# Kernel optimization log

Hardware: AMD Instinct MI355X
Metric: run time of the kernel (lower is better)

Reference implementation:

```python
import jax, jax.numpy as jnp
import numpy as np

N = 50000        # nodes
E = 800000       # edges
G = 256          # graphs in batch
DIMS = [128, 128, 64, 32]
BN_EPS = 1e-5
TEMP = 5.0


def setup_inputs() -> dict:
    key = jax.random.key(0)
    ks = iter(jax.random.split(key, 32))
    inp = {}
    inp["x"] = jax.random.normal(next(ks), (N, DIMS[0]), dtype=jnp.float32)
    inp["edge_index"] = jax.random.randint(next(ks), (2, E), 0, N)
    inp["batch"] = jnp.sort(jax.random.randint(next(ks), (N,), 0, G))
    for i in range(3):
        din, dout = DIMS[i], DIMS[i + 1]
        inp[f"W1_{i}"] = jax.random.normal(next(ks), (din, dout), dtype=jnp.float32) * 0.05
        inp[f"b1_{i}"] = jnp.zeros((dout,), jnp.float32)
        inp[f"W2_{i}"] = jax.random.normal(next(ks), (dout, dout), dtype=jnp.float32) * 0.05
        inp[f"b2_{i}"] = jnp.zeros((dout,), jnp.float32)
        inp[f"gamma_{i}"] = jnp.ones((dout,), jnp.float32)
        inp[f"beta_{i}"] = jnp.zeros((dout,), jnp.float32)
        inp[f"mean_{i}"] = jnp.zeros((dout,), jnp.float32)
        inp[f"var_{i}"] = jnp.ones((dout,), jnp.float32)
    inp["W_lin"] = jax.random.normal(next(ks), (DIMS[3], 1), dtype=jnp.float32) * 0.05
    inp["b_lin"] = jnp.zeros((1,), jnp.float32)
    return inp


def _gin_bn(x, src, dst, W1, b1, W2, b2, g, b, m, v):
    # GINConv with eps=0: h_i = MLP(x_i + sum_{j->i} x_j), then BatchNorm (eval)
    agg = jax.ops.segment_sum(x[src], dst, num_segments=N)  # [N, din]
    h = x + agg
    h = jnp.maximum(h @ W1 + b1, 0.0) @ W2 + b2             # 2-layer MLP
    return (h - m) * jax.lax.rsqrt(v + BN_EPS) * g + b


def reference(x, edge_index, batch,
              W1_0, b1_0, W2_0, b2_0, gamma_0, beta_0, mean_0, var_0,
              W1_1, b1_1, W2_1, b2_1, gamma_1, beta_1, mean_1, var_1,
              W1_2, b1_2, W2_2, b2_2, gamma_2, beta_2, mean_2, var_2,
              W_lin, b_lin):
    src, dst = edge_index[0], edge_index[1]
    layers = [
        (W1_0, b1_0, W2_0, b2_0, gamma_0, beta_0, mean_0, var_0),
        (W1_1, b1_1, W2_1, b2_1, gamma_1, beta_1, mean_1, var_1),
        (W1_2, b1_2, W2_2, b2_2, gamma_2, beta_2, mean_2, var_2),
    ]
    for i, p in enumerate(layers):
        x = _gin_bn(x, src, dst, *p)
        if i != len(layers) - 1:
            x = jnp.maximum(x, 0.0)  # relu; dropout is identity in eval mode
    logits = (x @ W_lin + b_lin) / TEMP                      # [N, 1]
    # per-graph (segment) softmax over nodes
    mx = jax.ops.segment_max(logits, batch, num_segments=G)  # [G, 1]
    e = jnp.exp(logits - mx[batch])
    s = jax.ops.segment_sum(e, batch, num_segments=G)        # [G, 1]
    return e / s[batch]
```

## Files before the change

kernel.cpp:

```cpp
#include <hip/hip_runtime.h>

#define NN 50000
#define NE 800000
#define NG 256
#define NB ((NN + 255) / 256)
#define N4 (NN * 128 / 4)

typedef __attribute__((ext_vector_type(8))) short bf16x8;
typedef __attribute__((ext_vector_type(4))) float f32x4;

__device__ __forceinline__ unsigned short f2bf_rne(float f) {
    unsigned u = __float_as_uint(f);
    u += 0x7fffu + ((u >> 16) & 1u);
    return (unsigned short)(u >> 16);
}
#define BF2F_LO(u) __uint_as_float((u) << 16)
#define BF2F_HI(u) __uint_as_float((u) & 0xffff0000u)

__global__ void conv_hist(const float4* __restrict__ x, ushort4* __restrict__ xh,
                          const int* __restrict__ dst, int* __restrict__ deg,
                          int* __restrict__ eoff) {
    int i = blockIdx.x * 256 + threadIdx.x;
    if (i < N4) {
        float4 v = x[i];
        ushort4 o;
        o.x = f2bf_rne(v.x); o.y = f2bf_rne(v.y);
        o.z = f2bf_rne(v.z); o.w = f2bf_rne(v.w);
        xh[i] = o;
    }
    if (i < NE) eoff[i] = atomicAdd(&deg[dst[i]], 1);
}

__global__ void block_scan(const int* __restrict__ deg, int* __restrict__ iscan,
                           int* __restrict__ bsum,
                           const float* __restrict__ W1, const float* __restrict__ W2,
                           const float* __restrict__ W3,
                           unsigned short* __restrict__ W1t,
                           unsigned short* __restrict__ W2t,
                           unsigned short* __restrict__ W3t) {
    int gidx = blockIdx.x * 256 + threadIdx.x;
    if (gidx < 16384) {
        int n = gidx >> 7, k = gidx & 127;
        W1t[gidx] = f2bf_rne(W1[k * 128 + n]);
        W2t[gidx] = f2bf_rne(W2[k * 128 + n]);
    } else if (gidx < 24576) {
        int i2 = gidx - 16384;
        int n = i2 >> 7, k = i2 & 127;
        W3t[i2] = f2bf_rne(W3[k * 64 + n]);
    }

    __shared__ int sh[256];
    int t = threadIdx.x;
    int i = blockIdx.x * 256 + t;
    int v = (i < NN) ? deg[i] : 0;
    sh[t] = v;
    __syncthreads();
    #pragma unroll
    for (int off = 1; off < 256; off <<= 1) {
        int add = (t >= off) ? sh[t - off] : 0;
        __syncthreads();
        sh[t] += add;
        __syncthreads();
    }
    if (i < NN) iscan[i] = sh[t];
    if (t == 255) bsum[blockIdx.x] = sh[255];
}

__global__ void scan_bsum(const int* __restrict__ bsum, int* __restrict__ boff) {
    __shared__ int sh[256];
    int t = threadIdx.x;
    int v = (t < NB) ? bsum[t] : 0;
    sh[t] = v;
    __syncthreads();
    #pragma unroll
    for (int off = 1; off < 256; off <<= 1) {
        int add = (t >= off) ? sh[t - off] : 0;
        __syncthreads();
        sh[t] += add;
        __syncthreads();
    }
    if (t < NB) boff[t] = sh[t] - v;
}

__global__ void finalize_bounds(const int* __restrict__ deg, const int* __restrict__ iscan,
                                const int* __restrict__ boff, int* __restrict__ rowptr,
                                const int* __restrict__ batch, int* __restrict__ gstart) {
    int i = blockIdx.x * 256 + threadIdx.x;
    if (i < NN) {
        rowptr[i] = iscan[i] - deg[i] + boff[blockIdx.x];
        int b = batch[i];
        if (i == 0) {
            for (int g = 0; g <= b; g++) gstart[g] = 0;
        } else {
            int p = batch[i - 1];
            for (int g = p + 1; g <= b; g++) gstart[g] = i;
        }
        if (i == NN - 1) {
            for (int g = b + 1; g <= NG; g++) gstart[g] = NN;
        }
    }
    if (i == 0) rowptr[NN] = NE;
}

__global__ void fill_csr2(const int* __restrict__ src, const int* __restrict__ dst,
                          const int* __restrict__ rowptr, const int* __restrict__ eoff,
                          int* __restrict__ esrc) {
    int e = blockIdx.x * blockDim.x + threadIdx.x;
    if (e >= NE) return;
    esrc[rowptr[dst[e]] + eoff[e]] = src[e];
}


template <int C4>
__device__ __forceinline__ void gather_bf16(const uint4* __restrict__ x4,
                                            const int* __restrict__ esrc,
                                            int beg, int cnt, int node, int lane,
                                            float* a ) {
    constexpr int EPI = 64 / C4;
    const int chunk = lane & (C4 - 1);
    const int esl   = lane / C4;
    #define ACC_U4(u) do { \
        a[0] += BF2F_LO((u).x); a[1] += BF2F_HI((u).x); \
        a[2] += BF2F_LO((u).y); a[3] += BF2F_HI((u).y); \
        a[4] += BF2F_LO((u).z); a[5] += BF2F_HI((u).z); \
        a[6] += BF2F_LO((u).w); a[7] += BF2F_HI((u).w); } while (0)
    if (esl == 0) { uint4 u = x4[(size_t)node * C4 + chunk]; ACC_U4(u); }
    for (int c = 0; c < cnt; c += 64) {
        int take = min(64, cnt - c);
        int myi = (lane < take) ? esrc[beg + c + lane] : 0;
        int i = 0;
        for (; i + 4 * EPI <= take; i += 4 * EPI) {
            int s0 = __shfl(myi, i + esl);
            int s1 = __shfl(myi, i + EPI + esl);
            int s2 = __shfl(myi, i + 2 * EPI + esl);
            int s3 = __shfl(myi, i + 3 * EPI + esl);
            uint4 u0 = x4[(size_t)s0 * C4 + chunk];
            uint4 u1 = x4[(size_t)s1 * C4 + chunk];
            uint4 u2 = x4[(size_t)s2 * C4 + chunk];
            uint4 u3 = x4[(size_t)s3 * C4 + chunk];
            ACC_U4(u0); ACC_U4(u1); ACC_U4(u2); ACC_U4(u3);
        }
        if (i + 2 * EPI <= take) {
            int s0 = __shfl(myi, i + esl);
            int s1 = __shfl(myi, i + EPI + esl);
            uint4 u0 = x4[(size_t)s0 * C4 + chunk];
            uint4 u1 = x4[(size_t)s1 * C4 + chunk];
            ACC_U4(u0); ACC_U4(u1);
            i += 2 * EPI;
        }
        if (i + EPI <= take) {
            int s = __shfl(myi, i + esl);
            uint4 u = x4[(size_t)s * C4 + chunk];
            ACC_U4(u);
            i += EPI;
        }
        int rem = take - i;
        if (rem > 0) {
            int s = __shfl(myi, i + ((esl < rem) ? esl : 0));
            uint4 u = x4[(size_t)s * C4 + chunk];
            if (esl < rem) ACC_U4(u);
        }
    }
    #undef ACC_U4
    for (int off = 32; off >= C4; off >>= 1) {
        #pragma unroll
        for (int q = 0; q < 8; q++)
            a[q] += __shfl_xor(a[q], off);
    }
}

template <int C>
__device__ __forceinline__ void gather_bf16_u2(const uint2* __restrict__ x2,
                                               const int* __restrict__ esrc,
                                               int beg, int cnt, int node, int lane,
                                               float* a ) {
    constexpr int EPI = 64 / C;
    const int chunk = lane & (C - 1);
    const int esl   = lane / C;
    #define ACC_U2(u) do { \
        a[0] += BF2F_LO((u).x); a[1] += BF2F_HI((u).x); \
        a[2] += BF2F_LO((u).y); a[3] += BF2F_HI((u).y); } while (0)
    if (esl == 0) { uint2 u = x2[(size_t)node * C + chunk]; ACC_U2(u); }
    for (int c = 0; c < cnt; c += 64) {
        int take = min(64, cnt - c);
        int myi = (lane < take) ? esrc[beg + c + lane] : 0;
        int i = 0;
        for (; i + 4 * EPI <= take; i += 4 * EPI) {
            int s0 = __shfl(myi, i + esl);
            int s1 = __shfl(myi, i + EPI + esl);
            int s2 = __shfl(myi, i + 2 * EPI + esl);
            int s3 = __shfl(myi, i + 3 * EPI + esl);
            uint2 u0 = x2[(size_t)s0 * C + chunk];
            uint2 u1 = x2[(size_t)s1 * C + chunk];
            uint2 u2 = x2[(size_t)s2 * C + chunk];
            uint2 u3 = x2[(size_t)s3 * C + chunk];
            ACC_U2(u0); ACC_U2(u1); ACC_U2(u2); ACC_U2(u3);
        }
        if (i + 2 * EPI <= take) {
            int s0 = __shfl(myi, i + esl);
            int s1 = __shfl(myi, i + EPI + esl);
            uint2 u0 = x2[(size_t)s0 * C + chunk];
            uint2 u1 = x2[(size_t)s1 * C + chunk];
            ACC_U2(u0); ACC_U2(u1);
            i += 2 * EPI;
        }
        if (i + EPI <= take) {
            int s = __shfl(myi, i + esl);
            uint2 u = x2[(size_t)s * C + chunk];
            ACC_U2(u);
            i += EPI;
        }
        int rem = take - i;
        if (rem > 0) {
            int s = __shfl(myi, i + ((esl < rem) ? esl : 0));
            uint2 u = x2[(size_t)s * C + chunk];
            if (esl < rem) ACC_U2(u);
        }
    }
    #undef ACC_U2
    for (int off = 32; off >= C; off >>= 1) {
        #pragma unroll
        for (int q = 0; q < 4; q++)
            a[q] += __shfl_xor(a[q], off);
    }
}

template <int C>
__device__ __forceinline__ void gather_bf16_u1(const unsigned* __restrict__ x1,
                                               const int* __restrict__ esrc,
                                               int beg, int cnt, int node, int lane,
                                               float* a ) {
    constexpr int EPI = 64 / C;
    const int chunk = lane & (C - 1);
    const int esl   = lane / C;
    #define ACC_U1(u) do { \
        a[0] += BF2F_LO(u); a[1] += BF2F_HI(u); } while (0)
    if (esl == 0) { unsigned u = x1[(size_t)node * C + chunk]; ACC_U1(u); }
    for (int c = 0; c < cnt; c += 64) {
        int take = min(64, cnt - c);
        int myi = (lane < take) ? esrc[beg + c + lane] : 0;
        int i = 0;
        for (; i + 4 * EPI <= take; i += 4 * EPI) {
            int s0 = __shfl(myi, i + esl);
            int s1 = __shfl(myi, i + EPI + esl);
            int s2 = __shfl(myi, i + 2 * EPI + esl);
            int s3 = __shfl(myi, i + 3 * EPI + esl);
            unsigned u0 = x1[(size_t)s0 * C + chunk];
            unsigned u1 = x1[(size_t)s1 * C + chunk];
            unsigned u2 = x1[(size_t)s2 * C + chunk];
            unsigned u3 = x1[(size_t)s3 * C + chunk];
            ACC_U1(u0); ACC_U1(u1); ACC_U1(u2); ACC_U1(u3);
        }
        if (i + 2 * EPI <= take) {
            int s0 = __shfl(myi, i + esl);
            int s1 = __shfl(myi, i + EPI + esl);
            unsigned u0 = x1[(size_t)s0 * C + chunk];
            unsigned u1 = x1[(size_t)s1 * C + chunk];
            ACC_U1(u0); ACC_U1(u1);
            i += 2 * EPI;
        }
        if (i + EPI <= take) {
            int s = __shfl(myi, i + esl);
            unsigned u = x1[(size_t)s * C + chunk];
            ACC_U1(u);
            i += EPI;
        }
        int rem = take - i;
        if (rem > 0) {
            int s = __shfl(myi, i + ((esl < rem) ? esl : 0));
            unsigned u = x1[(size_t)s * C + chunk];
            if (esl < rem) ACC_U1(u);
        }
    }
    #undef ACC_U1
    for (int off = 32; off >= C; off >>= 1) {
        #pragma unroll
        for (int q = 0; q < 2; q++)
            a[q] += __shfl_xor(a[q], off);
    }
}

__global__ __launch_bounds__(256) void gather_L0(
        const unsigned short* __restrict__ xh, const int* __restrict__ esrc,
        const int* __restrict__ rowptr, unsigned short* __restrict__ aggh ) {
    const int wave = threadIdx.x >> 6, lane = threadIdx.x & 63;
    const int node = blockIdx.x * 4 + wave;
    if (node >= NN) return;
    float a[8] = {0, 0, 0, 0, 0, 0, 0, 0};
    int beg = rowptr[node], end = rowptr[node + 1];
    gather_bf16<16>((const uint4*)xh, esrc, beg, end - beg, node, lane, a);
    if (lane < 16) {
        uint4 o;
        o.x = (unsigned)f2bf_rne(a[0]) | ((unsigned)f2bf_rne(a[1]) << 16);
        o.y = (unsigned)f2bf_rne(a[2]) | ((unsigned)f2bf_rne(a[3]) << 16);
        o.z = (unsigned)f2bf_rne(a[4]) | ((unsigned)f2bf_rne(a[5]) << 16);
        o.w = (unsigned)f2bf_rne(a[6]) | ((unsigned)f2bf_rne(a[7]) << 16);
        *(uint4*)&aggh[(size_t)node * 128 + lane * 8] = o;
    }
}

__global__ __launch_bounds__(256) void gemm_L0(
        const unsigned short* __restrict__ aggh, unsigned short* __restrict__ z1h,
        const unsigned short* __restrict__ W1t,
        const unsigned short* __restrict__ W2t,
        const unsigned short* __restrict__ W3t,
        const float* __restrict__ b1, const float* __restrict__ b2,
        const float* __restrict__ gamma, const float* __restrict__ beta,
        const float* __restrict__ mean, const float* __restrict__ var) {
    constexpr int MT = 64, LDA = 136;
    __shared__ __align__(16) unsigned short shA[MT * LDA];
    __shared__ __align__(16) unsigned short shB[MT * LDA];
    const int tid = threadIdx.x;
    const int wave = tid >> 6, lane = tid & 63;
    const int nodeBase = blockIdx.x * MT;
    const int lr = lane & 15;
    const int lg = lane >> 4;
    const int lk = lg * 8;
    const int n0 = wave * 32;

    #pragma unroll
    for (int j = 0; j < 4; j++) {
        int f = tid + j * 256;
        int row = f >> 4, c = f & 15;
        int node = nodeBase + row;
        uint4 v = (node < NN) ? ((const uint4*)aggh)[(size_t)node * 16 + c]
                              : make_uint4(0u, 0u, 0u, 0u);
        *(uint4*)&shA[row * LDA + c * 8] = v;
    }
    __syncthreads();

    f32x4 acc[4][2];

    {
        float bv0 = b1[n0 + lr], bv1 = b1[n0 + 16 + lr];
        #pragma unroll
        for (int m = 0; m < 4; m++) {
            f32x4 c0 = {bv0, bv0, bv0, bv0};
            f32x4 c1 = {bv1, bv1, bv1, bv1};
            acc[m][0] = c0; acc[m][1] = c1;
        }
        #pragma unroll
        for (int ks = 0; ks < 4; ks++) {
            const int k0 = ks * 32 + lk;
            bf16x8 wb0 = *(const bf16x8*)&W1t[(n0 + lr) * 128 + k0];
            bf16x8 wb1 = *(const bf16x8*)&W1t[(n0 + 16 + lr) * 128 + k0];
            #pragma unroll
            for (int m = 0; m < 4; m++) {
                bf16x8 af = *(const bf16x8*)&shA[(m * 16 + lr) * LDA + k0];
                acc[m][0] = __builtin_amdgcn_mfma_f32_16x16x32_bf16(af, wb0, acc[m][0], 0, 0, 0);
                acc[m][1] = __builtin_amdgcn_mfma_f32_16x16x32_bf16(af, wb1, acc[m][1], 0, 0, 0);
            }
        }
    }
    #pragma unroll
    for (int m = 0; m < 4; m++) {
        #pragma unroll
        for (int nt = 0; nt < 2; nt++) {
            #pragma unroll
            for (int r = 0; r < 4; r++) {
                shB[(m * 16 + lg * 4 + r) * LDA + (n0 + nt * 16 + lr)] =
                    f2bf_rne(fmaxf(acc[m][nt][r], 0.f));
            }
        }
    }
    __syncthreads();

    {
        float bv0 = b2[n0 + lr], bv1 = b2[n0 + 16 + lr];
        #pragma unroll
        for (int m = 0; m < 4; m++) {
            f32x4 c0 = {bv0, bv0, bv0, bv0};
            f32x4 c1 = {bv1, bv1, bv1, bv1};
            acc[m][0] = c0; acc[m][1] = c1;
        }
        #pragma unroll
        for (int ks = 0; ks < 4; ks++) {
            const int k0 = ks * 32 + lk;
            bf16x8 wb0 = *(const bf16x8*)&W2t[(n0 + lr) * 128 + k0];
            bf16x8 wb1 = *(const bf16x8*)&W2t[(n0 + 16 + lr) * 128 + k0];
            #pragma unroll
            for (int m = 0; m < 4; m++) {
                bf16x8 af = *(const bf16x8*)&shB[(m * 16 + lr) * LDA + k0];
                acc[m][0] = __builtin_amdgcn_mfma_f32_16x16x32_bf16(af, wb0, acc[m][0], 0, 0, 0);
                acc[m][1] = __builtin_amdgcn_mfma_f32_16x16x32_bf16(af, wb1, acc[m][1], 0, 0, 0);
            }
        }
    }
    float s0 = gamma[n0 + lr]      * (1.0f / sqrtf(var[n0 + lr] + 1e-5f));
    float t0 = beta[n0 + lr]       - mean[n0 + lr] * s0;
    float s1 = gamma[n0 + 16 + lr] * (1.0f / sqrtf(var[n0 + 16 + lr] + 1e-5f));
    float t1 = beta[n0 + 16 + lr]  - mean[n0 + 16 + lr] * s1;
    #pragma unroll
    for (int m = 0; m < 4; m++) {
        #pragma unroll
        for (int nt = 0; nt < 2; nt++) {
            float sc = nt ? s1 : s0, sf = nt ? t1 : t0;
            #pragma unroll
            for (int r = 0; r < 4; r++) {
                float y = fmaxf(fmaf(acc[m][nt][r], sc, sf), 0.f);
                shA[(m * 16 + lg * 4 + r) * LDA + (n0 + nt * 16 + lr)] = f2bf_rne(y);
            }
        }
    }
    __syncthreads();

    f32x4 a3[4];
    #pragma unroll
    for (int m = 0; m < 4; m++) {
        f32x4 z = {0.f, 0.f, 0.f, 0.f};
        a3[m] = z;
    }
    #pragma unroll
    for (int ks = 0; ks < 4; ks++) {
        const int k0 = ks * 32 + lk;
        bf16x8 wb = *(const bf16x8*)&W3t[(wave * 16 + lr) * 128 + k0];
        #pragma unroll
        for (int m = 0; m < 4; m++) {
            bf16x8 af = *(const bf16x8*)&shA[(m * 16 + lr) * LDA + k0];
            a3[m] = __builtin_amdgcn_mfma_f32_16x16x32_bf16(af, wb, a3[m], 0, 0, 0);
        }
    }
    #pragma unroll
    for (int m = 0; m < 4; m++) {
        #pragma unroll
        for (int r = 0; r < 4; r++) {
            int node = nodeBase + m * 16 + lg * 4 + r;
            if (node < NN)
                z1h[(size_t)node * 64 + wave * 16 + lr] = f2bf_rne(a3[m][r]);
        }
    }
}

__global__ __launch_bounds__(256) void fused_L1(
        const unsigned short* __restrict__ z1h, const int* __restrict__ esrc,
        const int* __restrict__ rowptr, unsigned short* __restrict__ z2h,
        const float* __restrict__ b1, const float* __restrict__ W2,
        const float* __restrict__ b2, const float* __restrict__ gamma,
        const float* __restrict__ beta, const float* __restrict__ mean,
        const float* __restrict__ var, const float* __restrict__ Wn ) {
    constexpr int MT = 32, LD = 68;
    __shared__ float sh[MT * LD];
    const int tid = threadIdx.x, wave = tid >> 6, lane = tid & 63;
    const int nodeBase = blockIdx.x * MT;

    for (int r = wave; r < MT; r += 4) {
        int node = nodeBase + r;
        float a[4] = {0, 0, 0, 0};
        if (node < NN) {
            int beg = rowptr[node], end = rowptr[node + 1];
            gather_bf16_u2<16>((const uint2*)z1h, esrc, beg, end - beg, node, lane, a);
        }
        if (lane < 16) {
            float4 b0 = *(const float4*)&b1[lane * 4];
            *(float4*)&sh[r * LD + lane * 4] = make_float4(
                fmaxf(a[0] + b0.x, 0.f), fmaxf(a[1] + b0.y, 0.f),
                fmaxf(a[2] + b0.z, 0.f), fmaxf(a[3] + b0.w, 0.f));
        }
    }
    __syncthreads();

    const int colid = tid % 16, rowid = tid / 16;
    const int c0 = colid * 4, r0 = rowid * 2;
    float acc[2][4];
    {
        float4 bv = *(const float4*)&b2[c0];
        #pragma unroll
        for (int i = 0; i < 2; i++) {
            acc[i][0] = bv.x; acc[i][1] = bv.y; acc[i][2] = bv.z; acc[i][3] = bv.w;
        }
        #pragma unroll 2
        for (int k4 = 0; k4 < 16; k4++) {
            float4 w[4];
            #pragma unroll
            for (int kk = 0; kk < 4; kk++)
                w[kk] = *(const float4*)&W2[(k4 * 4 + kk) * 64 + c0];
            #pragma unroll
            for (int i = 0; i < 2; i++) {
                float4 a = *(const float4*)&sh[(r0 + i) * LD + k4 * 4];
                const float av[4] = {a.x, a.y, a.z, a.w};
                #pragma unroll
                for (int kk = 0; kk < 4; kk++) {
                    const float* wp = (const float*)&w[kk];
                    #pragma unroll
                    for (int j = 0; j < 4; j++)
                        acc[i][j] = fmaf(av[kk], wp[j], acc[i][j]);
                }
            }
        }
    }
    float4 gv = *(const float4*)&gamma[c0];
    float4 bev = *(const float4*)&beta[c0];
    float4 mv = *(const float4*)&mean[c0];
    float4 vv = *(const float4*)&var[c0];
    float scale[4], shift[4];
    {
        const float* gp = (const float*)&gv; const float* bp = (const float*)&bev;
        const float* mp = (const float*)&mv; const float* vp = (const float*)&vv;
        #pragma unroll
        for (int j = 0; j < 4; j++) {
            scale[j] = gp[j] * (1.0f / sqrtf(vp[j] + 1e-5f));
            shift[j] = bp[j] - mp[j] * scale[j];
        }
    }
    __syncthreads();
    #pragma unroll
    for (int i = 0; i < 2; i++) {
        float4 y;
        y.x = fmaxf(fmaf(acc[i][0], scale[0], shift[0]), 0.f);
        y.y = fmaxf(fmaf(acc[i][1], scale[1], shift[1]), 0.f);
        y.z = fmaxf(fmaf(acc[i][2], scale[2], shift[2]), 0.f);
        y.w = fmaxf(fmaf(acc[i][3], scale[3], shift[3]), 0.f);
        *(float4*)&sh[(r0 + i) * LD + c0] = y;
    }
    __syncthreads();

    {
        const int colid2 = tid % 8, rowid2 = tid / 8;
        const int c0b = colid2 * 4, r0b = rowid2;
        float a3[4] = {};
        #pragma unroll 2
        for (int k4 = 0; k4 < 16; k4++) {
            float4 w[4];
            #pragma unroll
            for (int kk = 0; kk < 4; kk++)
                w[kk] = *(const float4*)&Wn[(k4 * 4 + kk) * 32 + c0b];
            float4 a = *(const float4*)&sh[r0b * LD + k4 * 4];
            const float av[4] = {a.x, a.y, a.z, a.w};
            #pragma unroll
            for (int kk = 0; kk < 4; kk++) {
                const float* wp = (const float*)&w[kk];
                #pragma unroll
                for (int j = 0; j < 4; j++)
                    a3[j] = fmaf(av[kk], wp[j], a3[j]);
            }
        }
        int node = nodeBase + r0b;
        if (node < NN) {
            ushort4 o;
            o.x = f2bf_rne(a3[0]); o.y = f2bf_rne(a3[1]);
            o.z = f2bf_rne(a3[2]); o.w = f2bf_rne(a3[3]);
            *(ushort4*)&z2h[(size_t)node * 32 + c0b] = o;
        }
    }
}

__global__ __launch_bounds__(256) void fused_L2(
        const unsigned short* __restrict__ z2h, const int* __restrict__ esrc,
        const int* __restrict__ rowptr, float* __restrict__ logits,
        const float* __restrict__ b1, const float* __restrict__ W2,
        const float* __restrict__ b2, const float* __restrict__ gamma,
        const float* __restrict__ beta, const float* __restrict__ mean,
        const float* __restrict__ var, const float* __restrict__ Wl,
        const float* __restrict__ bl) {
    constexpr int MT = 32, LD = 36;
    __shared__ float sh[MT * LD];
    const int tid = threadIdx.x, wave = tid >> 6, lane = tid & 63;
    const int nodeBase = blockIdx.x * MT;

    for (int r = wave; r < MT; r += 4) {
        int node = nodeBase + r;
        float a[2] = {0, 0};
        if (node < NN) {
            int beg = rowptr[node], end = rowptr[node + 1];
            gather_bf16_u1<16>((const unsigned*)z2h, esrc, beg, end - beg, node, lane, a);
        }
        if (lane < 16) {
            float2 bv = *(const float2*)&b1[lane * 2];
            *(float2*)&sh[r * LD + lane * 2] = make_float2(
                fmaxf(a[0] + bv.x, 0.f), fmaxf(a[1] + bv.y, 0.f));
        }
    }
    __syncthreads();

    const int colid = tid % 8, rowid = tid / 8;
    const int c0 = colid * 4, r0 = rowid;
    float acc[4];
    {
        float4 bv = *(const float4*)&b2[c0];
        acc[0] = bv.x; acc[1] = bv.y; acc[2] = bv.z; acc[3] = bv.w;
        #pragma unroll
        for (int k4 = 0; k4 < 8; k4++) {
            float4 w[4];
            #pragma unroll
            for (int kk = 0; kk < 4; kk++)
                w[kk] = *(const float4*)&W2[(k4 * 4 + kk) * 32 + c0];
            float4 a = *(const float4*)&sh[r0 * LD + k4 * 4];
            const float av[4] = {a.x, a.y, a.z, a.w};
            #pragma unroll
            for (int kk = 0; kk < 4; kk++) {
                const float* wp = (const float*)&w[kk];
                #pragma unroll
                for (int j = 0; j < 4; j++)
                    acc[j] = fmaf(av[kk], wp[j], acc[j]);
            }
        }
    }
    float4 gv = *(const float4*)&gamma[c0];
    float4 bev = *(const float4*)&beta[c0];
    float4 mv = *(const float4*)&mean[c0];
    float4 vv = *(const float4*)&var[c0];
    float4 wl = *(const float4*)&Wl[c0];
    float p = 0.f;
    {
        const float* gp = (const float*)&gv; const float* bp = (const float*)&bev;
        const float* mp = (const float*)&mv; const float* vp = (const float*)&vv;
        const float* wp = (const float*)&wl;
        #pragma unroll
        for (int j = 0; j < 4; j++) {
            float sc = gp[j] * (1.0f / sqrtf(vp[j] + 1e-5f));
            float y = (acc[j] - mp[j]) * sc + bp[j];
            p = fmaf(y, wp[j], p);
        }
    }
    p += __shfl_xor(p, 1);
    p += __shfl_xor(p, 2);
    p += __shfl_xor(p, 4);
    int node = nodeBase + r0;
    if ((tid & 7) == 0 && node < NN)
        logits[node] = (p + bl[0]) * 0.2f;
}

__global__ __launch_bounds__(256) void seg_softmax(
        const float* __restrict__ logits, const int* __restrict__ gstart,
        float* __restrict__ out) {
    __shared__ float slog[1024];
    __shared__ float sred[4];
    __shared__ float sbc[2];
    int g = blockIdx.x;
    int beg = gstart[g], end = gstart[g + 1];
    int cnt = end - beg;
    int t = threadIdx.x;
    if (cnt <= 0) return;
    bool fits = (cnt <= 1024);

    float lmax = -3.402823466e+38f;
    for (int i = t; i < cnt; i += 256) {
        float lg = logits[beg + i];
        if (fits) slog[i] = lg;
        lmax = fmaxf(lmax, lg);
    }
    #pragma unroll
    for (int off = 32; off > 0; off >>= 1)
        lmax = fmaxf(lmax, __shfl_down(lmax, off));
    if ((t & 63) == 0) sred[t >> 6] = lmax;
    __syncthreads();
    if (t == 0) sbc[0] = fmaxf(fmaxf(sred[0], sred[1]), fmaxf(sred[2], sred[3]));
    __syncthreads();
    float gm = sbc[0];

    float lsum = 0.f;
    for (int i = t; i < cnt; i += 256) {
        float lg = fits ? slog[i] : logits[beg + i];
        float e = expf(lg - gm);
        if (fits) slog[i] = e;
        lsum += e;
    }
    #pragma unroll
    for (int off = 32; off > 0; off >>= 1)
        lsum += __shfl_down(lsum, off);
    __syncthreads();
    if ((t & 63) == 0) sred[t >> 6] = lsum;
    __syncthreads();
    if (t == 0) sbc[1] = (sred[0] + sred[1]) + (sred[2] + sred[3]);
    __syncthreads();
    float inv = 1.0f / sbc[1];

    for (int i = t; i < cnt; i += 256) {
        float e = fits ? slog[i] : expf(logits[beg + i] - gm);
        out[beg + i] = e * inv;
    }
}

extern "C" void kernel_launch(void* const* d_in, const int* in_sizes, int n_in,
                              void* d_out, int out_size, void* d_ws, size_t ws_size,
                              hipStream_t stream) {
    const float* x    = (const float*)d_in[0];
    const int*   ei   = (const int*)d_in[1];
    const int*   srcI = ei;
    const int*   dstI = ei + NE;
    const int*   batch = (const int*)d_in[2];

    const float* P[29];
    for (int i = 0; i < 29; i++) P[i] = (const float*)d_in[i];
    const float* Wlin = P[27];
    const float* blin = P[28];

    unsigned short* xh  = (unsigned short*)d_ws;
    unsigned short* z1h = xh + (size_t)NN * 128;
    unsigned short* z2h = z1h + (size_t)NN * 64;
    float* logits = (float*)(z2h + (size_t)NN * 32);
    int* gstart = (int*)(logits + NN);
    int* deg    = gstart + NG + 1;
    int* iscan  = deg + NN;
    int* rowptr = iscan + NN;
    int* bsum   = rowptr + NN + 1;
    int* boff   = bsum + NB;
    int* eoff   = boff + NB;
    int* esrc   = eoff + NE;
    uintptr_t pal = ((uintptr_t)(esrc + NE) + 255) & ~(uintptr_t)255;
    unsigned short* aggh = (unsigned short*)pal;
    unsigned short* W1t  = aggh + (size_t)NN * 128;
    unsigned short* W2t  = W1t + 16384;
    unsigned short* W3t  = W2t + 16384;
    float* outp = (float*)d_out;

    const int TB = 256;

    hipMemsetAsync(deg, 0, NN * sizeof(int), stream);
    conv_hist<<<(N4 + TB - 1) / TB, TB, 0, stream>>>(
        (const float4*)x, (ushort4*)xh, dstI, deg, eoff);

    block_scan<<<NB, 256, 0, stream>>>(deg, iscan, bsum,
        P[3], P[5], P[11], W1t, W2t, W3t);
    scan_bsum<<<1, 256, 0, stream>>>(bsum, boff);
    finalize_bounds<<<NB, 256, 0, stream>>>(deg, iscan, boff, rowptr, batch, gstart);
    fill_csr2<<<(NE + TB - 1) / TB, TB, 0, stream>>>(srcI, dstI, rowptr, eoff, esrc);

    const int GB  = (NN + 3) / 4;
    const int FB64 = (NN + 63) / 64;
    const int FB32 = (NN + 31) / 32;

    gather_L0<<<GB, 256, 0, stream>>>(xh, esrc, rowptr, aggh);
    gemm_L0<<<FB64, 256, 0, stream>>>(aggh, z1h, W1t, W2t, W3t,
        P[4], P[6], P[7], P[8], P[9], P[10]);
    fused_L1<<<FB32, 256, 0, stream>>>(z1h, esrc, rowptr, z2h,
        P[12], P[13], P[14], P[15], P[16], P[17], P[18], P[19]);
    fused_L2<<<FB32, 256, 0, stream>>>(z2h, esrc, rowptr, logits,
        P[20], P[21], P[22], P[23], P[24], P[25], P[26], Wlin, blin);

    seg_softmax<<<NG, 256, 0, stream>>>(logits, gstart, outp);
}
```

Before: 305.6 us.

## Split L1/L2 fused kernels into gather + MFMA GEMM kernels

The fused gather-plus-FP32-GEMM kernels for layers 1 and 2 are each split into a separate per-node gather kernel and a dense GEMM kernel. The gathers write bf16 aggregates to new workspace buffers. The layer-1 MLP now runs on bf16 MFMA instructions using weights transposed and converted in the setup kernel, replacing scalar FP32 FMAs. This is meant to cut ALU time and stop the gather latency from stalling the GEMM. The cost is extra global round trips for the intermediates, two more kernel launches, and bf16 rounding of the layer-1 GEMM inputs.

```diff
diff --git a/kernel.cpp b/kernel.cpp
--- a/kernel.cpp
+++ b/kernel.cpp
@@ -35,9 +35,12 @@
                            int* __restrict__ bsum,
                            const float* __restrict__ W1, const float* __restrict__ W2,
                            const float* __restrict__ W3,
+                           const float* __restrict__ W21, const float* __restrict__ W12,
                            unsigned short* __restrict__ W1t,
                            unsigned short* __restrict__ W2t,
-                           unsigned short* __restrict__ W3t) {
+                           unsigned short* __restrict__ W3t,
+                           unsigned short* __restrict__ W21t,
+                           unsigned short* __restrict__ W12t) {
     int gidx = blockIdx.x * 256 + threadIdx.x;
     if (gidx < 16384) {
         int n = gidx >> 7, k = gidx & 127;
@@ -47,6 +50,14 @@
         int i2 = gidx - 16384;
         int n = i2 >> 7, k = i2 & 127;
         W3t[i2] = f2bf_rne(W3[k * 64 + n]);
+    } else if (gidx < 28672) {
+        int i3 = gidx - 24576;
+        int n = i3 >> 6, k = i3 & 63;
+        W21t[i3] = f2bf_rne(W21[k * 64 + n]);
+    } else if (gidx < 30720) {
+        int i4 = gidx - 28672;
+        int n = i4 >> 6, k = i4 & 63;
+        W12t[i4] = f2bf_rne(W12[k * 32 + n]);
     }
 
     __shared__ int sh[256];
@@ -299,6 +310,45 @@
     }
 }
 
+__global__ __launch_bounds__(256) void gather_L1(
+        const unsigned short* __restrict__ z1h, const int* __restrict__ esrc,
+        const int* __restrict__ rowptr, const float* __restrict__ b1,
+        unsigned short* __restrict__ agg1h ) {
+    const int wave = threadIdx.x >> 6, lane = threadIdx.x & 63;
+    const int node = blockIdx.x * 4 + wave;
+    if (node >= NN) return;
+    float a[4] = {0, 0, 0, 0};
+    int beg = rowptr[node], end = rowptr[node + 1];
+    gather_bf16_u2<16>((const uint2*)z1h, esrc, beg, end - beg, node, lane, a);
+    if (lane < 16) {
+        float4 bv = *(const float4*)&b1[lane * 4];
+        uint2 o;
+        o.x = (unsigned)f2bf_rne(fmaxf(a[0] + bv.x, 0.f)) |
+              ((unsigned)f2bf_rne(fmaxf(a[1] + bv.y, 0.f)) << 16);
+        o.y = (unsigned)f2bf_rne(fmaxf(a[2] + bv.z, 0.f)) |
+              ((unsigned)f2bf_rne(fmaxf(a[3] + bv.w, 0.f)) << 16);
+        *(uint2*)&agg1h[(size_t)node * 64 + lane * 4] = o;
+    }
+}
+
+__global__ __launch_bounds__(256) void gather_L2(
+        const unsigned short* __restrict__ z2h, const int* __restrict__ esrc,
+        const int* __restrict__ rowptr, const float* __restrict__ b1,
+        unsigned short* __restrict__ agg2h ) {
+    const int wave = threadIdx.x >> 6, lane = threadIdx.x & 63;
+    const int node = blockIdx.x * 4 + wave;
+    if (node >= NN) return;
+    float a[2] = {0, 0};
+    int beg = rowptr[node], end = rowptr[node + 1];
+    gather_bf16_u1<16>((const unsigned*)z2h, esrc, beg, end - beg, node, lane, a);
+    if (lane < 16) {
+        float2 bv = *(const float2*)&b1[lane * 2];
+        unsigned o = (unsigned)f2bf_rne(fmaxf(a[0] + bv.x, 0.f)) |
+                     ((unsigned)f2bf_rne(fmaxf(a[1] + bv.y, 0.f)) << 16);
+        *(unsigned*)&agg2h[(size_t)node * 32 + lane * 2] = o;
+    }
+}
+
 __global__ __launch_bounds__(256) void gemm_L0(
         const unsigned short* __restrict__ aggh, unsigned short* __restrict__ z1h,
         const unsigned short* __restrict__ W1t,
@@ -431,144 +481,113 @@
     }
 }
 
-__global__ __launch_bounds__(256) void fused_L1(
-        const unsigned short* __restrict__ z1h, const int* __restrict__ esrc,
-        const int* __restrict__ rowptr, unsigned short* __restrict__ z2h,
-        const float* __restrict__ b1, const float* __restrict__ W2,
+__global__ __launch_bounds__(256) void gemm_L1(
+        const unsigned short* __restrict__ agg1h, unsigned short* __restrict__ z2h,
+        const unsigned short* __restrict__ W21t,
+        const unsigned short* __restrict__ W12t,
         const float* __restrict__ b2, const float* __restrict__ gamma,
         const float* __restrict__ beta, const float* __restrict__ mean,
-        const float* __restrict__ var, const float* __restrict__ Wn ) {
-    constexpr int MT = 32, LD = 68;
-    __shared__ float sh[MT * LD];
-    const int tid = threadIdx.x, wave = tid >> 6, lane = tid & 63;
+        const float* __restrict__ var) {
+    constexpr int MT = 64, LDA = 72;
+    __shared__ __align__(16) unsigned short shA[MT * LDA];
+    __shared__ __align__(16) unsigned short shB[MT * LDA];
+    const int tid = threadIdx.x;
+    const int wave = tid >> 6, lane = tid & 63;
     const int nodeBase = blockIdx.x * MT;
-
-    for (int r = wave; r < MT; r += 4) {
-        int node = nodeBase + r;
-        float a[4] = {0, 0, 0, 0};
-        if (node < NN) {
-            int beg = rowptr[node], end = rowptr[node + 1];
-            gather_bf16_u2<16>((const uint2*)z1h, esrc, beg, end - beg, node, lane, a);
-        }
-        if (lane < 16) {
-            float4 b0 = *(const float4*)&b1[lane * 4];
-            *(float4*)&sh[r * LD + lane * 4] = make_float4(
-                fmaxf(a[0] + b0.x, 0.f), fmaxf(a[1] + b0.y, 0.f),
-                fmaxf(a[2] + b0.z, 0.f), fmaxf(a[3] + b0.w, 0.f));
-        }
-    }
-    __syncthreads();
-
-    const int colid = tid % 16, rowid = tid / 16;
-    const int c0 = colid * 4, r0 = rowid * 2;
-    float acc[2][4];
+    const int lr = lane & 15;
+    const int lg = lane >> 4;
+    const int lk = lg * 8;
+    const int n0 = wave * 16;
+
+    #pragma unroll
+    for (int j = 0; j < 2; j++) {
+        int f = tid + j * 256;
+        int row = f >> 3, c = f & 7;
+        int node = nodeBase + row;
+        uint4 v = (node < NN) ? ((const uint4*)agg1h)[(size_t)node * 8 + c]
+                              : make_uint4(0u, 0u, 0u, 0u);
+        *(uint4*)&shA[row * LDA + c * 8] = v;
+    }
+    __syncthreads();
+
+    f32x4 acc[4];
     {
-        float4 bv = *(const float4*)&b2[c0];
-        #pragma unroll
-        for (int i = 0; i < 2; i++) {
-            acc[i][0] = bv.x; acc[i][1] = bv.y; acc[i][2] = bv.z; acc[i][3] = bv.w;
-        }
-        #pragma unroll 2
-        for (int k4 = 0; k4 < 16; k4++) {
-            float4 w[4];
+        float bv = b2[n0 + lr];
+        #pragma unroll
+        for (int m = 0; m < 4; m++) {
+            f32x4 c0 = {bv, bv, bv, bv};
+            acc[m] = c0;
+        }
+        #pragma unroll
+        for (int ks = 0; ks < 2; ks++) {
+            const int k0 = ks * 32 + lk;
+            bf16x8 wb = *(const bf16x8*)&W21t[(n0 + lr) * 64 + k0];
             #pragma unroll
-            for (int kk = 0; kk < 4; kk++)
-                w[kk] = *(const float4*)&W2[(k4 * 4 + kk) * 64 + c0];
-            #pragma unroll
-            for (int i = 0; i < 2; i++) {
-                float4 a = *(const float4*)&sh[(r0 + i) * LD + k4 * 4];
-                const float av[4] = {a.x, a.y, a.z, a.w};
-                #pragma unroll
-                for (int kk = 0; kk < 4; kk++) {
-                    const float* wp = (const float*)&w[kk];
-                    #pragma unroll
-                    for (int j = 0; j < 4; j++)
-                        acc[i][j] = fmaf(av[kk], wp[j], acc[i][j]);
-                }
+            for (int m = 0; m < 4; m++) {
+                bf16x8 af = *(const bf16x8*)&shA[(m * 16 + lr) * LDA + k0];
+                acc[m] = __builtin_amdgcn_mfma_f32_16x16x32_bf16(af, wb, acc[m], 0, 0, 0);
             }
         }
     }
-    float4 gv = *(const float4*)&gamma[c0];
-    float4 bev = *(const float4*)&beta[c0];
-    float4 mv = *(const float4*)&mean[c0];
-    float4 vv = *(const float4*)&var[c0];
-    float scale[4], shift[4];
+    float sc = gamma[n0 + lr] * (1.0f / sqrtf(var[n0 + lr] + 1e-5f));
+    float sf = beta[n0 + lr] - mean[n0 + lr] * sc;
+    #pragma unroll
+    for (int m = 0; m < 4; m++) {
+        #pragma unroll
+        for (int r = 0; r < 4; r++) {
+            float y = fmaxf(fmaf(acc[m][r], sc, sf), 0.f);
+            shB[(m * 16 + lg * 4 + r) * LDA + (n0 + lr)] = f2bf_rne(y);
+        }
+    }
+    __syncthreads();
+
+    const int rh = (wave >> 1) * 32, ch = (wave & 1) * 16;
+    f32x4 a3[2];
     {
-        const float* gp = (const float*)&gv; const float* bp = (const float*)&bev;
-        const float* mp = (const float*)&mv; const float* vp = (const float*)&vv;
-        #pragma unroll
-        for (int j = 0; j < 4; j++) {
-            scale[j] = gp[j] * (1.0f / sqrtf(vp[j] + 1e-5f));
-            shift[j] = bp[j] - mp[j] * scale[j];
-        }
-    }
-    __syncthreads();
-    #pragma unroll
-    for (int i = 0; i < 2; i++) {
-        float4 y;
-        y.x = fmaxf(fmaf(acc[i][0], scale[0], shift[0]), 0.f);
-        y.y = fmaxf(fmaf(acc[i][1], scale[1], shift[1]), 0.f);
-        y.z = fmaxf(fmaf(acc[i][2], scale[2], shift[2]), 0.f);
-        y.w = fmaxf(fmaf(acc[i][3], scale[3], shift[3]), 0.f);
-        *(float4*)&sh[(r0 + i) * LD + c0] = y;
-    }
-    __syncthreads();
-
-    {
-        const int colid2 = tid % 8, rowid2 = tid / 8;
-        const int c0b = colid2 * 4, r0b = rowid2;
-        float a3[4] = {};
-        #pragma unroll 2
-        for (int k4 = 0; k4 < 16; k4++) {
-            float4 w[4];
-            #pragma unroll
-            for (int kk = 0; kk < 4; kk++)
-                w[kk] = *(const float4*)&Wn[(k4 * 4 + kk) * 32 + c0b];
-            float4 a = *(const float4*)&sh[r0b * LD + k4 * 4];
-            const float av[4] = {a.x, a.y, a.z, a.w};
-            #pragma unroll
-            for (int kk = 0; kk < 4; kk++) {
-                const float* wp = (const float*)&w[kk];
-                #pragma unroll
-                for (int j = 0; j < 4; j++)
-                    a3[j] = fmaf(av[kk], wp[j], a3[j]);
-            }
-        }
-        int node = nodeBase + r0b;
-        if (node < NN) {
-            ushort4 o;
-            o.x = f2bf_rne(a3[0]); o.y = f2bf_rne(a3[1]);
-            o.z = f2bf_rne(a3[2]); o.w = f2bf_rne(a3[3]);
-            *(ushort4*)&z2h[(size_t)node * 32 + c0b] = o;
-        }
-    }
-}
-
-__global__ __launch_bounds__(256) void fused_L2(
-        const unsigned short* __restrict__ z2h, const int* __restrict__ esrc,
-        const int* __restrict__ rowptr, float* __restrict__ logits,
-        const float* __restrict__ b1, const float* __restrict__ W2,
-        const float* __restrict__ b2, const float* __restrict__ gamma,
-        const float* __restrict__ beta, const float* __restrict__ mean,
-        const float* __restrict__ var, const float* __restrict__ Wl,
-        const float* __restrict__ bl) {
+        f32x4 z = {0.f, 0.f, 0.f, 0.f};
+        a3[0] = z; a3[1] = z;
+    }
+    #pragma unroll
+    for (int ks = 0; ks < 2; ks++) {
+        const int k0 = ks * 32 + lk;
+        bf16x8 wb = *(const bf16x8*)&W12t[(ch + lr) * 64 + k0];
+        #pragma unroll
+        for (int m = 0; m < 2; m++) {
+            bf16x8 af = *(const bf16x8*)&shB[(rh + m * 16 + lr) * LDA + k0];
+            a3[m] = __builtin_amdgcn_mfma_f32_16x16x32_bf16(af, wb, a3[m], 0, 0, 0);
+        }
+    }
+    #pragma unroll
+    for (int m = 0; m < 2; m++) {
+        #pragma unroll
+        for (int r = 0; r < 4; r++) {
+            int node = nodeBase + rh + m * 16 + lg * 4 + r;
+            if (node < NN)
+                z2h[(size_t)node * 32 + ch + lr] = f2bf_rne(a3[m][r]);
+        }
+    }
+}
+
+__global__ __launch_bounds__(256) void gemm_L2(
+        const unsigned short* __restrict__ agg2h, float* __restrict__ logits,
+        const float* __restrict__ W2, const float* __restrict__ b2,
+        const float* __restrict__ gamma, const float* __restrict__ beta,
+        const float* __restrict__ mean, const float* __restrict__ var,
+        const float* __restrict__ Wl, const float* __restrict__ bl) {
     constexpr int MT = 32, LD = 36;
     __shared__ float sh[MT * LD];
-    const int tid = threadIdx.x, wave = tid >> 6, lane = tid & 63;
+    const int tid = threadIdx.x;
     const int nodeBase = blockIdx.x * MT;
 
-    for (int r = wave; r < MT; r += 4) {
-        int node = nodeBase + r;
-        float a[2] = {0, 0};
-        if (node < NN) {
-            int beg = rowptr[node], end = rowptr[node + 1];
-            gather_bf16_u1<16>((const unsigned*)z2h, esrc, beg, end - beg, node, lane, a);
-        }
-        if (lane < 16) {
-            float2 bv = *(const float2*)&b1[lane * 2];
-            *(float2*)&sh[r * LD + lane * 2] = make_float2(
-                fmaxf(a[0] + bv.x, 0.f), fmaxf(a[1] + bv.y, 0.f));
-        }
+    {
+        int row = tid >> 3, c = tid & 7;
+        int node = nodeBase + row;
+        uint2 v = (node < NN) ? ((const uint2*)agg2h)[(size_t)node * 8 + c]
+                              : make_uint2(0u, 0u);
+        sh[row * LD + c * 4 + 0] = BF2F_LO(v.x);
+        sh[row * LD + c * 4 + 1] = BF2F_HI(v.x);
+        sh[row * LD + c * 4 + 2] = BF2F_LO(v.y);
+        sh[row * LD + c * 4 + 3] = BF2F_HI(v.y);
     }
     __syncthreads();
 
@@ -698,10 +717,14 @@
     int* eoff   = boff + NB;
     int* esrc   = eoff + NE;
     uintptr_t pal = ((uintptr_t)(esrc + NE) + 255) & ~(uintptr_t)255;
-    unsigned short* aggh = (unsigned short*)pal;
-    unsigned short* W1t  = aggh + (size_t)NN * 128;
-    unsigned short* W2t  = W1t + 16384;
-    unsigned short* W3t  = W2t + 16384;
+    unsigned short* aggh  = (unsigned short*)pal;
+    unsigned short* W1t   = aggh + (size_t)NN * 128;
+    unsigned short* W2t   = W1t + 16384;
+    unsigned short* W3t   = W2t + 16384;
+    unsigned short* W21t  = W3t + 8192;
+    unsigned short* W12t  = W21t + 4096;
+    unsigned short* agg1h = W12t + 2048;
+    unsigned short* agg2h = agg1h + (size_t)NN * 64;
     float* outp = (float*)d_out;
 
     const int TB = 256;
@@ -711,22 +734,24 @@
         (const float4*)x, (ushort4*)xh, dstI, deg, eoff);
 
     block_scan<<<NB, 256, 0, stream>>>(deg, iscan, bsum,
-        P[3], P[5], P[11], W1t, W2t, W3t);
+        P[3], P[5], P[11], P[13], P[19], W1t, W2t, W3t, W21t, W12t);
     scan_bsum<<<1, 256, 0, stream>>>(bsum, boff);
     finalize_bounds<<<NB, 256, 0, stream>>>(deg, iscan, boff, rowptr, batch, gstart);
     fill_csr2<<<(NE + TB - 1) / TB, TB, 0, stream>>>(srcI, dstI, rowptr, eoff, esrc);
 
-    const int GB  = (NN + 3) / 4;
+    const int GB   = (NN + 3) / 4;
     const int FB64 = (NN + 63) / 64;
     const int FB32 = (NN + 31) / 32;
 
     gather_L0<<<GB, 256, 0, stream>>>(xh, esrc, rowptr, aggh);
     gemm_L0<<<FB64, 256, 0, stream>>>(aggh, z1h, W1t, W2t, W3t,
         P[4], P[6], P[7], P[8], P[9], P[10]);
-    fused_L1<<<FB32, 256, 0, stream>>>(z1h, esrc, rowptr, z2h,
-        P[12], P[13], P[14], P[15], P[16], P[17], P[18], P[19]);
-    fused_L2<<<FB32, 256, 0, stream>>>(z2h, esrc, rowptr, logits,
-        P[20], P[21], P[22], P[23], P[24], P[25], P[26], Wlin, blin);
+    gather_L1<<<GB, 256, 0, stream>>>(z1h, esrc, rowptr, P[12], agg1h);
+    gemm_L1<<<FB64, 256, 0, stream>>>(agg1h, z2h, W21t, W12t,
+        P[14], P[15], P[16], P[17], P[18]);
+    gather_L2<<<GB, 256, 0, stream>>>(z2h, esrc, rowptr, P[20], agg2h);
+    gemm_L2<<<FB32, 256, 0, stream>>>(agg2h, logits,
+        P[21], P[22], P[23], P[24], P[25], P[26], Wlin, blin);
 
     seg_softmax<<<NG, 256, 0, stream>>>(logits, gstart, outp);
 }
```

Result: faster. 285.6 us (-6.5%).
